# Optimization experiments

Hardware: AMD Instinct MI355X
Metric: run time of the kernel (lower is better)

The kernel has to match this reference:

```python
import jax, jax.numpy as jnp
import numpy as np

N_NODES = 50000
N_EDGES = 1600000
EMB = 128
HID = 128
OUT = 128
HEADS = 4
BN_EPS = 1e-5


def segment_softmax(e, seg, n):
    # numerically-stable softmax over variable-degree neighborhoods
    m = jax.ops.segment_max(e, seg, num_segments=n)
    m = jnp.where(jnp.isfinite(m), m, 0.0)
    ex = jnp.exp(e - m[seg])
    s = jax.ops.segment_sum(ex, seg, num_segments=n)
    return ex / (s[seg] + 1e-16)


def gat_layer(x, src, dst, W, att_src, att_dst, bias, concat):
    # PyG GATConv (eval mode, self-loops already added to src/dst)
    N = x.shape[0]
    H, C = att_src.shape
    h = (x @ W).reshape(N, H, C)                       # [N,H,C]
    a_src = jnp.einsum('nhc,hc->nh', h, att_src)       # [N,H]
    a_dst = jnp.einsum('nhc,hc->nh', h, att_dst)
    e = jax.nn.leaky_relu(a_src[src] + a_dst[dst], 0.2)  # [E,H]
    alpha = segment_softmax(e, dst, N)                 # [E,H]
    out = jax.ops.segment_sum(h[src] * alpha[:, :, None], dst, num_segments=N)
    out = out.reshape(N, H * C) if concat else out.mean(axis=1)
    return out + bias


def setup_inputs() -> dict:
    key = jax.random.key(0)
    ks = jax.random.split(key, 16)
    C1 = HID // HEADS
    inp = {
        'node_embeddings': jax.random.normal(ks[0], (N_NODES, EMB), jnp.float32),
        'edge_index': jax.random.randint(ks[1], (2, N_EDGES), 0, N_NODES, jnp.int64),
        'proj_W': jax.random.normal(ks[2], (EMB, HID), jnp.float32) * 0.05,
        'proj_b': jnp.zeros((HID,), jnp.float32),
        'W1': jax.random.normal(ks[3], (HID, HEADS * C1), jnp.float32) * 0.05,
        'att_src1': jax.random.normal(ks[4], (HEADS, C1), jnp.float32) * 0.05,
        'att_dst1': jax.random.normal(ks[5], (HEADS, C1), jnp.float32) * 0.05,
        'bias1': jnp.zeros((HEADS * C1,), jnp.float32),
        'bn_gamma': jnp.ones((HID,), jnp.float32),
        'bn_beta': jnp.zeros((HID,), jnp.float32),
        'W2': jax.random.normal(ks[6], (HID, HEADS * OUT), jnp.float32) * 0.05,
        'att_src2': jax.random.normal(ks[7], (HEADS, OUT), jnp.float32) * 0.05,
        'att_dst2': jax.random.normal(ks[8], (HEADS, OUT), jnp.float32) * 0.05,
        'bias2': jnp.zeros((OUT,), jnp.float32),
        'out_W': jax.random.normal(ks[9], (OUT, OUT), jnp.float32) * 0.05,
        'out_b': jnp.zeros((OUT,), jnp.float32),
    }
    return inp


def reference(node_embeddings, edge_index, proj_W, proj_b,
              W1, att_src1, att_dst1, bias1, bn_gamma, bn_beta,
              W2, att_src2, att_dst2, bias2, out_W, out_b):
    N = node_embeddings.shape[0]
    # add self-loops (PyG GATConv default)
    loops = jnp.arange(N, dtype=edge_index.dtype)
    src = jnp.concatenate([edge_index[0], loops])
    dst = jnp.concatenate([edge_index[1], loops])

    x = jax.nn.relu(node_embeddings @ proj_W + proj_b)
    x = gat_layer(x, src, dst, W1, att_src1, att_dst1, bias1, concat=True)
    # BatchNorm1d in eval mode: running_mean=0, running_var=1
    x = x / jnp.sqrt(1.0 + BN_EPS) * bn_gamma + bn_beta
    x = jax.nn.elu(x)
    # dropout is identity in eval mode
    x = gat_layer(x, src, dst, W2, att_src2, att_dst2, bias2, concat=False)
    x = x.mean(axis=0, keepdims=True)                  # [1, OUT]
    x = jax.nn.relu(x @ out_W + out_b)
    return x
```

## Files before the change

kernel.cpp:

```cpp
#include <hip/hip_runtime.h>
#include <hip/hip_bf16.h>

#define NN 50000
#define NROW 50048
#define NE 1600000
#define ETOT (NE + NN)
#define BN_K 0.9999950000374997f

#define SHIFT 7
#define NPB 128
#define NB ((NN + NPB - 1) >> SHIFT)
#define CAP 5120
#define CHUNK 4096
#define PGRID ((ETOT + CHUNK - 1) / CHUNK)
#define CVB (NROW * 32 / 256)

typedef __bf16 bf16x8 __attribute__((ext_vector_type(8)));
typedef float f32x4 __attribute__((ext_vector_type(4)));

__device__ __forceinline__ float leaky02(float x) { return x > 0.f ? x : 0.2f * x; }

__device__ __forceinline__ unsigned short f2bf(float f) {
    unsigned int u = __float_as_uint(f);
    u += 0x7FFFu + ((u >> 16) & 1u);
    return (unsigned short)(u >> 16);
}

__global__ void init_k(int* __restrict__ bcur_d, int* __restrict__ bcur_s,
                       float* __restrict__ y) {
    int t = threadIdx.x;
    if (t < NB) { bcur_d[t] = t * CAP; bcur_s[t] = t * CAP; }
    y[t] = 0.f;
}

__global__ void cvtw_k(const float* __restrict__ x0, unsigned short* __restrict__ x0b,
                       const float* __restrict__ pW, const float* __restrict__ W1,
                       unsigned short* __restrict__ pWt, unsigned short* __restrict__ W1t,
                       const float* __restrict__ W2, const float* __restrict__ as2,
                       const float* __restrict__ ad2, float* __restrict__ va_s,
                       float* __restrict__ va_d) {
    int b = blockIdx.x;
    if (b < CVB) {
        int g = b * 256 + threadIdx.x;
        int row = g >> 5;
        float4 v = make_float4(0.f, 0.f, 0.f, 0.f);
        if (row < NN) v = *(const float4*)&x0[(long)g * 4];
        ushort4 u;
        u.x = f2bf(v.x); u.y = f2bf(v.y); u.z = f2bf(v.z); u.w = f2bf(v.w);
        *(ushort4*)&x0b[(long)g * 4] = u;
    } else if (b < CVB + 2) {
        const float* in = (b - CVB) ? W1 : pW;
        unsigned short* outp = (b - CVB) ? W1t : pWt;
        for (int i = threadIdx.x; i < 16384; i += 256) {
            int n = i & 127, k = i >> 7;
            outp[n * 128 + k] = f2bf(in[k * 128 + n]);
        }
    } else {
        int h = b - CVB - 2;
        int k = threadIdx.x;
        if (k < 128) {
            const float* wrow = W2 + (long)k * 512 + h * 128;
            float accs = 0.f, accd = 0.f;
            for (int ci = 0; ci < 128; ++ci) {
                float w = wrow[ci];
                accs += w * as2[h * 128 + ci];
                accd += w * ad2[h * 128 + ci];
            }
            va_s[h * 128 + k] = accs;
            va_d[h * 128 + k] = accd;
        }
    }
}

__global__ __launch_bounds__(256) void fgemm_k(
    const unsigned short* __restrict__ x0b, const unsigned short* __restrict__ pWt,
    const unsigned short* __restrict__ W1t, const float* __restrict__ pb,
    const float* __restrict__ attS, const float* __restrict__ attD,
    unsigned short* __restrict__ h1b, float* __restrict__ aS, float* __restrict__ aD) {
    __shared__ unsigned short x1s[128][136];
    const int tid = threadIdx.x;
    const int wv = tid >> 6, l = tid & 63;
    const int lr = l & 15, lg = l >> 4;
    const int r0 = blockIdx.x * 128;
    const int wr = wv * 32;

    bf16x8 Af[2][4];
    f32x4 acc[2][8];

    #pragma unroll
    for (int rt = 0; rt < 2; ++rt)
        #pragma unroll
        for (int kt = 0; kt < 4; ++kt)
            Af[rt][kt] = *(const bf16x8*)&x0b[(long)(r0 + wr + rt * 16 + lr) * 128 + kt * 32 + lg * 8];
    #pragma unroll
    for (int rt = 0; rt < 2; ++rt)
        #pragma unroll
        for (int ct = 0; ct < 8; ++ct)
            acc[rt][ct] = (f32x4){0.f, 0.f, 0.f, 0.f};
    #pragma unroll
    for (int ct = 0; ct < 8; ++ct) {
        bf16x8 Bf[4];
        #pragma unroll
        for (int kt = 0; kt < 4; ++kt)
            Bf[kt] = *(const bf16x8*)&pWt[(ct * 16 + lr) * 128 + kt * 32 + lg * 8];
        #pragma unroll
        for (int kt = 0; kt < 4; ++kt) {
            acc[0][ct] = __builtin_amdgcn_mfma_f32_16x16x32_bf16(Af[0][kt], Bf[kt], acc[0][ct], 0, 0, 0);
            acc[1][ct] = __builtin_amdgcn_mfma_f32_16x16x32_bf16(Af[1][kt], Bf[kt], acc[1][ct], 0, 0, 0);
        }
    }
    #pragma unroll
    for (int ct = 0; ct < 8; ++ct) {
        int col = ct * 16 + lr;
        float bv = pb[col];
        #pragma unroll
        for (int rt = 0; rt < 2; ++rt)
            #pragma unroll
            for (int r = 0; r < 4; ++r) {
                float v = acc[rt][ct][r] + bv;
                x1s[wr + rt * 16 + lg * 4 + r][col] = f2bf(v > 0.f ? v : 0.f);
            }
    }
    __syncthreads();

    #pragma unroll
    for (int rt = 0; rt < 2; ++rt)
        #pragma unroll
        for (int kt = 0; kt < 4; ++kt)
            Af[rt][kt] = *(const bf16x8*)&x1s[wr + rt * 16 + lr][kt * 32 + lg * 8];
    #pragma unroll
    for (int rt = 0; rt < 2; ++rt)
        #pragma unroll
        for (int ct = 0; ct < 8; ++ct)
            acc[rt][ct] = (f32x4){0.f, 0.f, 0.f, 0.f};
    #pragma unroll
    for (int ct = 0; ct < 8; ++ct) {
        bf16x8 Bf[4];
        #pragma unroll
        for (int kt = 0; kt < 4; ++kt)
            Bf[kt] = *(const bf16x8*)&W1t[(ct * 16 + lr) * 128 + kt * 32 + lg * 8];
        #pragma unroll
        for (int kt = 0; kt < 4; ++kt) {
            acc[0][ct] = __builtin_amdgcn_mfma_f32_16x16x32_bf16(Af[0][kt], Bf[kt], acc[0][ct], 0, 0, 0);
            acc[1][ct] = __builtin_amdgcn_mfma_f32_16x16x32_bf16(Af[1][kt], Bf[kt], acc[1][ct], 0, 0, 0);
        }
    }
    __syncthreads();
    #pragma unroll
    for (int ct = 0; ct < 8; ++ct)
        #pragma unroll
        for (int rt = 0; rt < 2; ++rt)
            #pragma unroll
            for (int r = 0; r < 4; ++r)
                x1s[wr + rt * 16 + lg * 4 + r][ct * 16 + lr] = f2bf(acc[rt][ct][r]);
    __syncthreads();

    #pragma unroll
    for (int i = 0; i < 8; ++i) {
        int idx = tid + i * 256;
        int row = idx >> 4, cc = idx & 15;
        bf16x8 hv = *(const bf16x8*)&x1s[row][cc * 8];
        *(bf16x8*)&h1b[(long)(r0 + row) * 128 + cc * 8] = hv;
        int head = cc >> 2, lc = (cc & 3) * 8;
        float ps = 0.f, pd = 0.f;
        #pragma unroll
        for (int j = 0; j < 8; ++j) {
            float v = (float)hv[j];
            ps += v * attS[head * 32 + lc + j];
            pd += v * attD[head * 32 + lc + j];
        }
        ps += __shfl_xor(ps, 1); ps += __shfl_xor(ps, 2);
        pd += __shfl_xor(pd, 1); pd += __shfl_xor(pd, 2);
        if ((cc & 3) == 0) {
            aS[(r0 + row) * 4 + head] = ps;
            aD[(r0 + row) * 4 + head] = pd;
        }
    }
}

__global__ void part_k(const int* __restrict__ srcA, const int* __restrict__ dstA,
                       int* __restrict__ bcur_d, int* __restrict__ bcur_s,
                       int* __restrict__ pr_d, int* __restrict__ pr_s) {
    __shared__ int hd[NB], hs[NB], bd[NB], bs[NB];
    for (int i = threadIdx.x; i < NB; i += 256) { hd[i] = 0; hs[i] = 0; }
    __syncthreads();
    int e0 = blockIdx.x * CHUNK;
    int e1 = min(e0 + CHUNK, ETOT);
    for (int e = e0 + threadIdx.x; e < e1; e += 256) {
        int s, d;
        if (e < NE) { s = srcA[e]; d = dstA[e]; } else { s = d = e - NE; }
        atomicAdd(&hd[d >> SHIFT], 1);
        atomicAdd(&hs[s >> SHIFT], 1);
    }
    __syncthreads();
    for (int i = threadIdx.x; i < NB; i += 256) {
        if (hd[i]) { bd[i] = atomicAdd(&bcur_d[i], hd[i]); hd[i] = 0; }
        if (hs[i]) { bs[i] = atomicAdd(&bcur_s[i], hs[i]); hs[i] = 0; }
    }
    __syncthreads();
    for (int e = e0 + threadIdx.x; e < e1; e += 256) {
        int s, d;
        if (e < NE) { s = srcA[e]; d = dstA[e]; } else { s = d = e - NE; }
        int kd = d >> SHIFT;
        pr_d[bd[kd] + atomicAdd(&hd[kd], 1)] = ((d & (NPB - 1)) << 16) | s;
        int ks = s >> SHIFT;
        pr_s[bs[ks] + atomicAdd(&hs[ks], 1)] = ((s & (NPB - 1)) << 16) | d;
    }
}

__global__ void fine_k(const int* __restrict__ pr, const int* __restrict__ bcur,
                       int2* __restrict__ oe, int* __restrict__ csr) {
    __shared__ int cnt[NPB], off[NPB];
    int bkt = blockIdx.x;
    int n0 = bkt << SHIFT;
    int base = bkt * CAP, end = bcur[bkt];
    int t = threadIdx.x;
    if (t < NPB) cnt[t] = 0;
    __syncthreads();
    for (int i = base + t; i < end; i += 256)
        atomicAdd(&cnt[pr[i] >> 16], 1);
    __syncthreads();
    if (t < NPB) off[t] = cnt[t];
    __syncthreads();
    for (int dd = 1; dd < NPB; dd <<= 1) {
        int y = 0;
        if (t < NPB && t >= dd) y = off[t - dd];
        __syncthreads();
        if (t < NPB) off[t] += y;
        __syncthreads();
    }
    if (t < NPB) {
        int excl = off[t] - cnt[t];
        int n = n0 + t;
        if (n < NN) oe[n] = make_int2(base + excl, cnt[t]);
        off[t] = excl;
        cnt[t] = 0;
    }
    __syncthreads();
    for (int i = base + t; i < end; i += 256) {
        int p = pr[i];
        int j = p >> 16;
        int pos = base + off[j] + atomicAdd(&cnt[j], 1);
        csr[pos] = p & 0xFFFF;
    }
}

__global__ void gather1_k(const int* __restrict__ csr_src, const int2* __restrict__ oe_d,
                          const float* __restrict__ aS, const float* __restrict__ aD,
                          const unsigned short* __restrict__ h1b, const float* __restrict__ b1,
                          const float* __restrict__ bg, const float* __restrict__ bb,
                          const float* __restrict__ va_s, const float* __restrict__ va_d,
                          unsigned short* __restrict__ x2b, float* __restrict__ aS2,
                          float* __restrict__ aD2) {
    __shared__ float4 wst[4][64];
    __shared__ unsigned sst[4][64];
    int wv = threadIdx.x >> 6;
    int d = (blockIdx.x << 2) + wv;
    if (d >= NN) return;
    int lane = threadIdx.x & 63;
    float4 ad4 = *(const float4*)&aD[d * 4];
    int2 oe = oe_d[d];
    int o0 = oe.x, deg = oe.y, o1 = o0 + deg;

    float s0 = 0.f, s1 = 0.f, s2 = 0.f, s3 = 0.f;
    for (int base = o0; base < o1; base += 64) {
        int e = base + lane;
        if (e < o1) {
            int s = csr_src[e];
            float4 as4 = *(const float4*)&aS[s * 4];
            float4 w;
            w.x = __expf(leaky02(as4.x + ad4.x));
            w.y = __expf(leaky02(as4.y + ad4.y));
            w.z = __expf(leaky02(as4.z + ad4.z));
            w.w = __expf(leaky02(as4.w + ad4.w));
            wst[wv][lane] = w;
            sst[wv][lane] = (unsigned)(s << 8);
            s0 += w.x; s1 += w.y; s2 += w.z; s3 += w.w;
        }
    }
    #pragma unroll
    for (int off = 32; off; off >>= 1) {
        s0 += __shfl_xor(s0, off);
        s1 += __shfl_xor(s1, off);
        s2 += __shfl_xor(s2, off);
        s3 += __shfl_xor(s3, off);
    }
    float i0 = 1.f / (s0 + 1e-16f), i1 = 1.f / (s1 + 1e-16f);
    float i2 = 1.f / (s2 + 1e-16f), i3 = 1.f / (s3 + 1e-16f);

    int k = lane & 31, half = lane >> 5;
    unsigned cb = (unsigned)(k * 8);
    int headk = k >> 3;
    const char* h1base = (const char*)h1b;
    float a0 = 0.f, a1 = 0.f, a2 = 0.f, a3 = 0.f;

    if (deg <= 64) {
        if (lane < deg) {
            float4 w = wst[wv][lane];
            w.x *= i0; w.y *= i1; w.z *= i2; w.w *= i3;
            wst[wv][lane] = w;
        }
        __threadfence_block();
        for (int t = half; t < deg; t += 2) {
            float w = ((const float*)&wst[wv][t])[headk];
            unsigned ro = sst[wv][t];
            uint2 hv = *(const uint2*)(h1base + ro + cb);
            a0 += w * __uint_as_float(hv.x << 16);
            a1 += w * __uint_as_float(hv.x & 0xFFFF0000u);
            a2 += w * __uint_as_float(hv.y << 16);
            a3 += w * __uint_as_float(hv.y & 0xFFFF0000u);
        }
    } else {
        for (int base = o0; base < o1; base += 64) {
            int e = base + lane;
            if (e < o1) {
                int s = csr_src[e];
                float4 as4 = *(const float4*)&aS[s * 4];
                float4 w;
                w.x = __expf(leaky02(as4.x + ad4.x)) * i0;
                w.y = __expf(leaky02(as4.y + ad4.y)) * i1;
                w.z = __expf(leaky02(as4.z + ad4.z)) * i2;
                w.w = __expf(leaky02(as4.w + ad4.w)) * i3;
                wst[wv][lane] = w;
                sst[wv][lane] = (unsigned)(s << 8);
            }
            __threadfence_block();
            int nst = min(64, o1 - base);
            for (int t = half; t < nst; t += 2) {
                float w = ((const float*)&wst[wv][t])[headk];
                unsigned ro = sst[wv][t];
                uint2 hv = *(const uint2*)(h1base + ro + cb);
                a0 += w * __uint_as_float(hv.x << 16);
                a1 += w * __uint_as_float(hv.x & 0xFFFF0000u);
                a2 += w * __uint_as_float(hv.y << 16);
                a3 += w * __uint_as_float(hv.y & 0xFFFF0000u);
            }
            __threadfence_block();
        }
    }
    a0 += __shfl_xor(a0, 32); a1 += __shfl_xor(a1, 32);
    a2 += __shfl_xor(a2, 32); a3 += __shfl_xor(a3, 32);

    int c = k * 4;
    float v0 = (a0 + b1[c])     * BN_K * bg[c]     + bb[c];
    float v1 = (a1 + b1[c + 1]) * BN_K * bg[c + 1] + bb[c + 1];
    float v2 = (a2 + b1[c + 2]) * BN_K * bg[c + 2] + bb[c + 2];
    float v3 = (a3 + b1[c + 3]) * BN_K * bg[c + 3] + bb[c + 3];
    v0 = v0 > 0.f ? v0 : __expf(v0) - 1.f;
    v1 = v1 > 0.f ? v1 : __expf(v1) - 1.f;
    v2 = v2 > 0.f ? v2 : __expf(v2) - 1.f;
    v3 = v3 > 0.f ? v3 : __expf(v3) - 1.f;
    if (half == 0) {
        uint2 pk;
        pk.x = (unsigned)f2bf(v0) | ((unsigned)f2bf(v1) << 16);
        pk.y = (unsigned)f2bf(v2) | ((unsigned)f2bf(v3) << 16);
        *(uint2*)&x2b[(long)d * 128 + c] = pk;
    }

    float r[8];
    #pragma unroll
    for (int h = 0; h < 4; ++h) {
        float4 vs = *(const float4*)&va_s[h * 128 + c];
        float4 vd = *(const float4*)&va_d[h * 128 + c];
        float rs = v0 * vs.x + v1 * vs.y + v2 * vs.z + v3 * vs.w;
        float rd = v0 * vd.x + v1 * vd.y + v2 * vd.z + v3 * vd.w;
        r[h]     = half ? 0.f : rs;
        r[4 + h] = half ? 0.f : rd;
    }
    #pragma unroll
    for (int off = 32; off; off >>= 1) {
        #pragma unroll
        for (int j = 0; j < 8; ++j) r[j] += __shfl_xor(r[j], off);
    }
    if (lane == 0) {
        *(float4*)&aS2[d * 4] = make_float4(r[0], r[1], r[2], r[3]);
        *(float4*)&aD2[d * 4] = make_float4(r[4], r[5], r[6], r[7]);
    }
}

__global__ __launch_bounds__(512) void dsum2_k(const int* __restrict__ pr_d,
                                               const int* __restrict__ bcur_d,
                                               const float* __restrict__ aS2,
                                               const float* __restrict__ aD2,
                                               float* __restrict__ adL) {
    __shared__ float ad2s[NPB][4];
    __shared__ float sums[NPB * 4];
    int bkt = blockIdx.x, t = threadIdx.x;
    int n0 = bkt << SHIFT;
    sums[t] = 0.f;
    if (t < NPB) {
        int n = n0 + t;
        float4 v = (n < NN) ? *(const float4*)&aD2[n * 4] : make_float4(0.f, 0.f, 0.f, 0.f);
        *(float4*)&ad2s[t][0] = v;
    }
    __syncthreads();
    int base = bkt * CAP, end = bcur_d[bkt];
    for (int i = base + t; i < end; i += 512) {
        int p = pr_d[i];
        int ld = p >> 16, s = p & 0xFFFF;
        float4 as4 = *(const float4*)&aS2[s * 4];
        float4 adv = *(const float4*)&ad2s[ld][0];
        atomicAdd(&sums[ld * 4 + 0], __expf(leaky02(as4.x + adv.x)));
        atomicAdd(&sums[ld * 4 + 1], __expf(leaky02(as4.y + adv.y)));
        atomicAdd(&sums[ld * 4 + 2], __expf(leaky02(as4.z + adv.z)));
        atomicAdd(&sums[ld * 4 + 3], __expf(leaky02(as4.w + adv.w)));
    }
    __syncthreads();
    if (t < NPB) {
        int n = n0 + t;
        if (n < NN) {
            *(float4*)&adL[n * 8] = *(float4*)&ad2s[t][0];
            *(float4*)&adL[n * 8 + 4] = make_float4(
                1.f / (sums[t * 4 + 0] + 1e-16f), 1.f / (sums[t * 4 + 1] + 1e-16f),
                1.f / (sums[t * 4 + 2] + 1e-16f), 1.f / (sums[t * 4 + 3] + 1e-16f));
        }
    }
}

__global__ __launch_bounds__(512) void waccg2_k(const int* __restrict__ pr_s,
                                                const int* __restrict__ bcur_s,
                                                const float* __restrict__ aS2,
                                                const float* __restrict__ adL,
                                                float* __restrict__ Wacc) {
    __shared__ float as2s[NPB][4];
    __shared__ float wac[NPB * 4];
    int bkt = blockIdx.x, t = threadIdx.x;
    int n0 = bkt << SHIFT;
    wac[t] = 0.f;
    if (t < NPB) {
        int n = n0 + t;
        float4 v = (n < NN) ? *(const float4*)&aS2[n * 4] : make_float4(0.f, 0.f, 0.f, 0.f);
        *(float4*)&as2s[t][0] = v;
    }
    __syncthreads();
    int base = bkt * CAP, end = bcur_s[bkt];
    for (int i = base + t; i < end; i += 512) {
        int p = pr_s[i];
        int ls = p >> 16, d = p & 0xFFFF;
        float4 adv = *(const float4*)&adL[d * 8];
        float4 iv  = *(const float4*)&adL[d * 8 + 4];
        float4 asv = *(const float4*)&as2s[ls][0];
        atomicAdd(&wac[ls * 4 + 0], __expf(leaky02(asv.x + adv.x)) * iv.x);
        atomicAdd(&wac[ls * 4 + 1], __expf(leaky02(asv.y + adv.y)) * iv.y);
        atomicAdd(&wac[ls * 4 + 2], __expf(leaky02(asv.z + adv.z)) * iv.z);
        atomicAdd(&wac[ls * 4 + 3], __expf(leaky02(asv.w + adv.w)) * iv.w);
    }
    __syncthreads();
    if (t < NPB) {
        int n = n0 + t;
        if (n < NN) {
            const float scale = 0.25f / (float)NN;
            *(float4*)&Wacc[n * 4] = make_float4(scale * wac[t * 4 + 0], scale * wac[t * 4 + 1],
                                                 scale * wac[t * 4 + 2], scale * wac[t * 4 + 3]);
        }
    }
}

__global__ void yacc_k(const float* __restrict__ Wacc, const unsigned short* __restrict__ x2b,
                       float* __restrict__ y) {
    int k2 = threadIdx.x;
    float a[8] = {};
    for (int r = blockIdx.x; r < NN; r += gridDim.x) {
        float4 w = *(const float4*)&Wacc[r * 4];
        unsigned hv = *(const unsigned*)&x2b[(long)r * 128 + k2 * 2];
        float xl = __uint_as_float(hv << 16);
        float xh = __uint_as_float(hv & 0xFFFF0000u);
        a[0] += w.x * xl; a[1] += w.x * xh;
        a[2] += w.y * xl; a[3] += w.y * xh;
        a[4] += w.z * xl; a[5] += w.z * xh;
        a[6] += w.w * xl; a[7] += w.w * xh;
    }
    int c = k2 * 2;
    atomicAdd(&y[0 * 128 + c], a[0]); atomicAdd(&y[0 * 128 + c + 1], a[1]);
    atomicAdd(&y[1 * 128 + c], a[2]); atomicAdd(&y[1 * 128 + c + 1], a[3]);
    atomicAdd(&y[2 * 128 + c], a[4]); atomicAdd(&y[2 * 128 + c + 1], a[5]);
    atomicAdd(&y[3 * 128 + c], a[6]); atomicAdd(&y[3 * 128 + c + 1], a[7]);
}

__global__ void final2_k(const float* __restrict__ y, const float* __restrict__ W2,
                         const float* __restrict__ b2, const float* __restrict__ oW,
                         const float* __restrict__ ob, float* __restrict__ out) {
    __shared__ float xm[128];
    int c = threadIdx.x;
    float t = b2[c];
    #pragma unroll
    for (int h = 0; h < 4; ++h) {
        const float* yh = y + h * 128;
        for (int k = 0; k < 128; ++k) t += yh[k] * W2[(long)k * 512 + h * 128 + c];
    }
    xm[c] = t;
    __syncthreads();
    float acc = ob[c];
    for (int k = 0; k < 128; ++k) acc += xm[k] * oW[k * 128 + c];
    out[c] = acc > 0.f ? acc : 0.f;
}

extern "C" void kernel_launch(void* const* d_in, const int* in_sizes, int n_in,
                              void* d_out, int out_size, void* d_ws, size_t ws_size,
                              hipStream_t stream) {
    const float* x0  = (const float*)d_in[0];
    const int*   ei  = (const int*)d_in[1];
    const float* pW  = (const float*)d_in[2];
    const float* pb  = (const float*)d_in[3];
    const float* W1  = (const float*)d_in[4];
    const float* as1 = (const float*)d_in[5];
    const float* ad1 = (const float*)d_in[6];
    const float* b1  = (const float*)d_in[7];
    const float* bg  = (const float*)d_in[8];
    const float* bb  = (const float*)d_in[9];
    const float* W2  = (const float*)d_in[10];
    const float* as2 = (const float*)d_in[11];
    const float* ad2 = (const float*)d_in[12];
    const float* b2  = (const float*)d_in[13];
    const float* oW  = (const float*)d_in[14];
    const float* ob  = (const float*)d_in[15];
    float* out = (float*)d_out;

    float* ws = (float*)d_ws;
    unsigned short* x0b = (unsigned short*)ws; ws += 3203072;
    unsigned short* h1b = (unsigned short*)ws; ws += 3203072;
    unsigned short* x2b = (unsigned short*)ws; ws += 3200000;
    unsigned short* pWt = (unsigned short*)ws; ws += 8192;
    unsigned short* W1t = (unsigned short*)ws; ws += 8192;
    float* aS1   = ws; ws += 200192;
    float* aD1   = ws; ws += 200192;
    float* aS2   = ws; ws += 200000;
    float* aD2   = ws; ws += 200000;
    float* adL   = ws; ws += 400000;
    float* Wacc  = ws; ws += 200000;
    float* va_s  = ws; ws += 512;
    float* va_d  = ws; ws += 512;
    float* y     = ws; ws += 512;
    int* bcur_d  = (int*)ws; ws += NB;
    int* bcur_s  = (int*)ws; ws += NB;
    int2* oe_d   = (int2*)ws; ws += 2 * NN;
    int* csr_src = (int*)ws; ws += NB * CAP;
    int* pr_d    = (int*)ws; ws += NB * CAP;
    int* pr_s    = (int*)ws; ws += NB * CAP;

    const int* srcA = ei;
    const int* dstA = ei + NE;

    dim3 blk(256);

    init_k<<<1, 512, 0, stream>>>(bcur_d, bcur_s, y);
    cvtw_k<<<CVB + 6, blk, 0, stream>>>(x0, x0b, pW, W1, pWt, W1t, W2, as2, ad2, va_s, va_d);
    part_k<<<PGRID, blk, 0, stream>>>(srcA, dstA, bcur_d, bcur_s, pr_d, pr_s);
    fine_k<<<NB, blk, 0, stream>>>(pr_d, bcur_d, oe_d, csr_src);

    fgemm_k<<<NB, blk, 0, stream>>>(x0b, pWt, W1t, pb, as1, ad1, h1b, aS1, aD1);

    gather1_k<<<12500, blk, 0, stream>>>(csr_src, oe_d, aS1, aD1, h1b, b1, bg, bb,
                                         va_s, va_d, x2b, aS2, aD2);

    dsum2_k<<<NB, 512, 0, stream>>>(pr_d, bcur_d, aS2, aD2, adL);
    waccg2_k<<<NB, 512, 0, stream>>>(pr_s, bcur_s, aS2, adL, Wacc);
    yacc_k<<<256, 64, 0, stream>>>(Wacc, x2b, y);
    final2_k<<<1, 128, 0, stream>>>(y, W2, b2, oW, ob, out);
}
```

Baseline: 459.5 us.

## Build source-side CSR and replace LDS-atomic layer-2 reductions with per-node wave reductions

The partition kernel now stages each chunk's bucketed entries in shared memory via a local prefix scan, so writes to the global bucket arrays are grouped by bucket instead of scattered one by one. The fine sort also builds a source-keyed CSR alongside the destination one. The layer-2 softmax-denominator and weight-accumulation kernels then walk these CSRs with one wave per node and reduce through shuffles, replacing shared-memory float atomics over bucketed pairs. The cost is an extra CSR pass plus more workspace, and low-degree nodes leave many lanes of each wave idle.

```diff
diff --git a/kernel.cpp b/kernel.cpp
--- a/kernel.cpp
+++ b/kernel.cpp
@@ -178,42 +178,73 @@
     }
 }
 
-__global__ void part_k(const int* __restrict__ srcA, const int* __restrict__ dstA,
-                       int* __restrict__ bcur_d, int* __restrict__ bcur_s,
-                       int* __restrict__ pr_d, int* __restrict__ pr_s) {
-    __shared__ int hd[NB], hs[NB], bd[NB], bs[NB];
-    for (int i = threadIdx.x; i < NB; i += 256) { hd[i] = 0; hs[i] = 0; }
-    __syncthreads();
+__global__ __launch_bounds__(512) void part_k(const int* __restrict__ srcA,
+                                              const int* __restrict__ dstA,
+                                              int* __restrict__ bcur_d, int* __restrict__ bcur_s,
+                                              int* __restrict__ pr_d, int* __restrict__ pr_s) {
+    __shared__ int cnt[NB], gb[NB], lo[NB];
+    __shared__ int scanbuf[512];
+    __shared__ int stg[CHUNK];
+    __shared__ int dbuf[CHUNK];
+    int t = threadIdx.x;
     int e0 = blockIdx.x * CHUNK;
     int e1 = min(e0 + CHUNK, ETOT);
-    for (int e = e0 + threadIdx.x; e < e1; e += 256) {
-        int s, d;
-        if (e < NE) { s = srcA[e]; d = dstA[e]; } else { s = d = e - NE; }
-        atomicAdd(&hd[d >> SHIFT], 1);
-        atomicAdd(&hs[s >> SHIFT], 1);
-    }
-    __syncthreads();
-    for (int i = threadIdx.x; i < NB; i += 256) {
-        if (hd[i]) { bd[i] = atomicAdd(&bcur_d[i], hd[i]); hd[i] = 0; }
-        if (hs[i]) { bs[i] = atomicAdd(&bcur_s[i], hs[i]); hs[i] = 0; }
-    }
-    __syncthreads();
-    for (int e = e0 + threadIdx.x; e < e1; e += 256) {
-        int s, d;
-        if (e < NE) { s = srcA[e]; d = dstA[e]; } else { s = d = e - NE; }
-        int kd = d >> SHIFT;
-        pr_d[bd[kd] + atomicAdd(&hd[kd], 1)] = ((d & (NPB - 1)) << 16) | s;
-        int ks = s >> SHIFT;
-        pr_s[bs[ks] + atomicAdd(&hs[ks], 1)] = ((s & (NPB - 1)) << 16) | d;
-    }
-}
-
-__global__ void fine_k(const int* __restrict__ pr, const int* __restrict__ bcur,
-                       int2* __restrict__ oe, int* __restrict__ csr) {
+    #pragma unroll
+    for (int it = 0; it < 2; ++it) {
+        int* bcur = it ? bcur_s : bcur_d;
+        int* pr   = it ? pr_s   : pr_d;
+        for (int i = t; i < NB; i += 512) cnt[i] = 0;
+        __syncthreads();
+        for (int e = e0 + t; e < e1; e += 512) {
+            int s, d;
+            if (e < NE) { s = srcA[e]; d = dstA[e]; } else { s = d = e - NE; }
+            atomicAdd(&cnt[(it ? s : d) >> SHIFT], 1);
+        }
+        __syncthreads();
+        for (int i = t; i < NB; i += 512)
+            if (cnt[i]) gb[i] = atomicAdd(&bcur[i], cnt[i]);
+        scanbuf[t] = (t < NB) ? cnt[t] : 0;
+        __syncthreads();
+        for (int dd = 1; dd < 512; dd <<= 1) {
+            int y = (t >= dd) ? scanbuf[t - dd] : 0;
+            __syncthreads();
+            scanbuf[t] += y;
+            __syncthreads();
+        }
+        if (t < NB) lo[t] = scanbuf[t] - cnt[t];
+        __syncthreads();
+        if (t < NB) cnt[t] = lo[t];
+        __syncthreads();
+        for (int e = e0 + t; e < e1; e += 512) {
+            int s, d;
+            if (e < NE) { s = srcA[e]; d = dstA[e]; } else { s = d = e - NE; }
+            int n = it ? s : d, pay = it ? d : s;
+            int key = n >> SHIFT;
+            int idx = atomicAdd(&cnt[key], 1);
+            stg[idx]  = ((n & (NPB - 1)) << 16) | pay;
+            dbuf[idx] = gb[key] + (idx - lo[key]);
+        }
+        __syncthreads();
+        int tot = e1 - e0;
+        for (int p = t; p < tot; p += 512)
+            pr[dbuf[p]] = stg[p];
+        __syncthreads();
+    }
+}
+
+__global__ void fine_k(const int* __restrict__ pr_d, const int* __restrict__ bcur_d,
+                       int2* __restrict__ oe_d, int* __restrict__ csr_src,
+                       const int* __restrict__ pr_s, const int* __restrict__ bcur_s,
+                       int2* __restrict__ oe_s, int* __restrict__ csr_dst) {
+    bool dk = blockIdx.x < NB;
+    const int* pr    = dk ? pr_d : pr_s;
+    const int* bcurb = dk ? bcur_d : bcur_s;
+    int2* oe         = dk ? oe_d : oe_s;
+    int* csr         = dk ? csr_src : csr_dst;
+    int bkt = dk ? blockIdx.x : blockIdx.x - NB;
     __shared__ int cnt[NPB], off[NPB];
-    int bkt = blockIdx.x;
     int n0 = bkt << SHIFT;
-    int base = bkt * CAP, end = bcur[bkt];
+    int base = bkt * CAP, end = bcurb[bkt];
     int t = threadIdx.x;
     if (t < NPB) cnt[t] = 0;
     __syncthreads();
@@ -378,81 +409,67 @@
     }
 }
 
-__global__ __launch_bounds__(512) void dsum2_k(const int* __restrict__ pr_d,
-                                               const int* __restrict__ bcur_d,
-                                               const float* __restrict__ aS2,
-                                               const float* __restrict__ aD2,
-                                               float* __restrict__ adL) {
-    __shared__ float ad2s[NPB][4];
-    __shared__ float sums[NPB * 4];
-    int bkt = blockIdx.x, t = threadIdx.x;
-    int n0 = bkt << SHIFT;
-    sums[t] = 0.f;
-    if (t < NPB) {
-        int n = n0 + t;
-        float4 v = (n < NN) ? *(const float4*)&aD2[n * 4] : make_float4(0.f, 0.f, 0.f, 0.f);
-        *(float4*)&ad2s[t][0] = v;
-    }
-    __syncthreads();
-    int base = bkt * CAP, end = bcur_d[bkt];
-    for (int i = base + t; i < end; i += 512) {
-        int p = pr_d[i];
-        int ld = p >> 16, s = p & 0xFFFF;
-        float4 as4 = *(const float4*)&aS2[s * 4];
-        float4 adv = *(const float4*)&ad2s[ld][0];
-        atomicAdd(&sums[ld * 4 + 0], __expf(leaky02(as4.x + adv.x)));
-        atomicAdd(&sums[ld * 4 + 1], __expf(leaky02(as4.y + adv.y)));
-        atomicAdd(&sums[ld * 4 + 2], __expf(leaky02(as4.z + adv.z)));
-        atomicAdd(&sums[ld * 4 + 3], __expf(leaky02(as4.w + adv.w)));
-    }
-    __syncthreads();
-    if (t < NPB) {
-        int n = n0 + t;
-        if (n < NN) {
-            *(float4*)&adL[n * 8] = *(float4*)&ad2s[t][0];
-            *(float4*)&adL[n * 8 + 4] = make_float4(
-                1.f / (sums[t * 4 + 0] + 1e-16f), 1.f / (sums[t * 4 + 1] + 1e-16f),
-                1.f / (sums[t * 4 + 2] + 1e-16f), 1.f / (sums[t * 4 + 3] + 1e-16f));
-        }
-    }
-}
-
-__global__ __launch_bounds__(512) void waccg2_k(const int* __restrict__ pr_s,
-                                                const int* __restrict__ bcur_s,
-                                                const float* __restrict__ aS2,
-                                                const float* __restrict__ adL,
-                                                float* __restrict__ Wacc) {
-    __shared__ float as2s[NPB][4];
-    __shared__ float wac[NPB * 4];
-    int bkt = blockIdx.x, t = threadIdx.x;
-    int n0 = bkt << SHIFT;
-    wac[t] = 0.f;
-    if (t < NPB) {
-        int n = n0 + t;
-        float4 v = (n < NN) ? *(const float4*)&aS2[n * 4] : make_float4(0.f, 0.f, 0.f, 0.f);
-        *(float4*)&as2s[t][0] = v;
-    }
-    __syncthreads();
-    int base = bkt * CAP, end = bcur_s[bkt];
-    for (int i = base + t; i < end; i += 512) {
-        int p = pr_s[i];
-        int ls = p >> 16, d = p & 0xFFFF;
-        float4 adv = *(const float4*)&adL[d * 8];
+__global__ void dsum_k(const int* __restrict__ csr_src, const int2* __restrict__ oe_d,
+                       const float* __restrict__ aS, const float* __restrict__ aD,
+                       float* __restrict__ adL) {
+    int d = (blockIdx.x << 2) + (threadIdx.x >> 6);
+    if (d >= NN) return;
+    int lane = threadIdx.x & 63;
+    float4 ad4 = *(const float4*)&aD[d * 4];
+    int2 oe = oe_d[d];
+    int o0 = oe.x, o1 = oe.x + oe.y;
+    float s0 = 0.f, s1 = 0.f, s2 = 0.f, s3 = 0.f;
+    for (int o = o0 + lane; o < o1; o += 64) {
+        int s = csr_src[o];
+        float4 as4 = *(const float4*)&aS[s * 4];
+        s0 += __expf(leaky02(as4.x + ad4.x));
+        s1 += __expf(leaky02(as4.y + ad4.y));
+        s2 += __expf(leaky02(as4.z + ad4.z));
+        s3 += __expf(leaky02(as4.w + ad4.w));
+    }
+    #pragma unroll
+    for (int off = 32; off; off >>= 1) {
+        s0 += __shfl_xor(s0, off);
+        s1 += __shfl_xor(s1, off);
+        s2 += __shfl_xor(s2, off);
+        s3 += __shfl_xor(s3, off);
+    }
+    if (lane == 0) {
+        *(float4*)&adL[d * 8]     = ad4;
+        *(float4*)&adL[d * 8 + 4] = make_float4(1.f / (s0 + 1e-16f), 1.f / (s1 + 1e-16f),
+                                                1.f / (s2 + 1e-16f), 1.f / (s3 + 1e-16f));
+    }
+}
+
+__global__ void waccg_k(const int* __restrict__ csr_dst, const int2* __restrict__ oe_s,
+                        const float* __restrict__ aS, const float* __restrict__ adL,
+                        float* __restrict__ Wacc) {
+    int s = (blockIdx.x << 2) + (threadIdx.x >> 6);
+    if (s >= NN) return;
+    int lane = threadIdx.x & 63;
+    float4 as4 = *(const float4*)&aS[s * 4];
+    int2 oe = oe_s[s];
+    int o0 = oe.x, o1 = oe.x + oe.y;
+    float a0 = 0.f, a1 = 0.f, a2 = 0.f, a3 = 0.f;
+    for (int o = o0 + lane; o < o1; o += 64) {
+        int d = csr_dst[o];
+        float4 ad4 = *(const float4*)&adL[d * 8];
         float4 iv  = *(const float4*)&adL[d * 8 + 4];
-        float4 asv = *(const float4*)&as2s[ls][0];
-        atomicAdd(&wac[ls * 4 + 0], __expf(leaky02(asv.x + adv.x)) * iv.x);
-        atomicAdd(&wac[ls * 4 + 1], __expf(leaky02(asv.y + adv.y)) * iv.y);
-        atomicAdd(&wac[ls * 4 + 2], __expf(leaky02(asv.z + adv.z)) * iv.z);
-        atomicAdd(&wac[ls * 4 + 3], __expf(leaky02(asv.w + adv.w)) * iv.w);
-    }
-    __syncthreads();
-    if (t < NPB) {
-        int n = n0 + t;
-        if (n < NN) {
-            const float scale = 0.25f / (float)NN;
-            *(float4*)&Wacc[n * 4] = make_float4(scale * wac[t * 4 + 0], scale * wac[t * 4 + 1],
-                                                 scale * wac[t * 4 + 2], scale * wac[t * 4 + 3]);
-        }
+        a0 += __expf(leaky02(as4.x + ad4.x)) * iv.x;
+        a1 += __expf(leaky02(as4.y + ad4.y)) * iv.y;
+        a2 += __expf(leaky02(as4.z + ad4.z)) * iv.z;
+        a3 += __expf(leaky02(as4.w + ad4.w)) * iv.w;
+    }
+    #pragma unroll
+    for (int off = 32; off; off >>= 1) {
+        a0 += __shfl_xor(a0, off);
+        a1 += __shfl_xor(a1, off);
+        a2 += __shfl_xor(a2, off);
+        a3 += __shfl_xor(a3, off);
+    }
+    if (lane == 0) {
+        const float scale = 0.25f / (float)NN;
+        *(float4*)&Wacc[s * 4] = make_float4(scale * a0, scale * a1, scale * a2, scale * a3);
     }
 }
 
@@ -534,7 +551,9 @@
     int* bcur_d  = (int*)ws; ws += NB;
     int* bcur_s  = (int*)ws; ws += NB;
     int2* oe_d   = (int2*)ws; ws += 2 * NN;
+    int2* oe_s   = (int2*)ws; ws += 2 * NN;
     int* csr_src = (int*)ws; ws += NB * CAP;
+    int* csr_dst = (int*)ws; ws += NB * CAP;
     int* pr_d    = (int*)ws; ws += NB * CAP;
     int* pr_s    = (int*)ws; ws += NB * CAP;
 
@@ -545,16 +564,17 @@
 
     init_k<<<1, 512, 0, stream>>>(bcur_d, bcur_s, y);
     cvtw_k<<<CVB + 6, blk, 0, stream>>>(x0, x0b, pW, W1, pWt, W1t, W2, as2, ad2, va_s, va_d);
-    part_k<<<PGRID, blk, 0, stream>>>(srcA, dstA, bcur_d, bcur_s, pr_d, pr_s);
-    fine_k<<<NB, blk, 0, stream>>>(pr_d, bcur_d, oe_d, csr_src);
+    part_k<<<PGRID, 512, 0, stream>>>(srcA, dstA, bcur_d, bcur_s, pr_d, pr_s);
+    fine_k<<<2 * NB, blk, 0, stream>>>(pr_d, bcur_d, oe_d, csr_src,
+                                       pr_s, bcur_s, oe_s, csr_dst);
 
     fgemm_k<<<NB, blk, 0, stream>>>(x0b, pWt, W1t, pb, as1, ad1, h1b, aS1, aD1);
 
     gather1_k<<<12500, blk, 0, stream>>>(csr_src, oe_d, aS1, aD1, h1b, b1, bg, bb,
                                          va_s, va_d, x2b, aS2, aD2);
 
-    dsum2_k<<<NB, 512, 0, stream>>>(pr_d, bcur_d, aS2, aD2, adL);
-    waccg2_k<<<NB, 512, 0, stream>>>(pr_s, bcur_s, aS2, adL, Wacc);
+    dsum_k<<<12500, blk, 0, stream>>>(csr_src, oe_d, aS2, aD2, adL);
+    waccg_k<<<12500, blk, 0, stream>>>(csr_dst, oe_s, aS2, adL, Wacc);
     yacc_k<<<256, 64, 0, stream>>>(Wacc, x2b, y);
     final2_k<<<1, 128, 0, stream>>>(y, W2, b2, oW, ob, out);
 }
```

Result: faster. 396.8 us (-13.6%).
